# Optimization experiments

Measured on AMD Instinct MI355X. Metric: run time of the kernel, lower is better.

The kernel has to match this reference:

```python
import jax, jax.numpy as jnp
import numpy as np

DIM = 512
NUM_LATENTS = 128
TRUE_BATCH = 8
DOWNSCALING = 16


def setup_inputs() -> dict:
    key = jax.random.key(0)
    ks = jax.random.split(key, 7)
    B = TRUE_BATCH * NUM_LATENTS
    s = 0.02
    return {
        "x": jax.random.normal(ks[0], (B, DOWNSCALING, DIM), dtype=jnp.float32),
        "l": jax.random.normal(ks[1], (B, NUM_LATENTS, DIM), dtype=jnp.float32),
        "Wq": jax.random.normal(ks[2], (DIM, DIM), dtype=jnp.float32) * s,
        "Wk": jax.random.normal(ks[3], (DIM, DIM), dtype=jnp.float32) * s,
        "Wv": jax.random.normal(ks[4], (DIM, DIM), dtype=jnp.float32) * s,
        "Wo": jax.random.normal(ks[5], (DIM, DIM), dtype=jnp.float32) * s,
        "bo": jax.random.normal(ks[6], (DIM,), dtype=jnp.float32) * s,
        "num_heads": 8,
    }


def reference(x, l, Wq, Wk, Wv, Wo, bo, num_heads):
    B, n_tok, d = x.shape
    num_latents = l.shape[1]
    dh = d // num_heads

    def split_heads(t):
        # (b, n, h*d) -> (b, h, n, d)
        b, n, _ = t.shape
        return t.reshape(b, n, num_heads, dh).transpose(0, 2, 1, 3)

    q = split_heads(x @ Wq.T)   # (B, h, n_tok, dh)
    k = split_heads(l @ Wk.T)   # (B, h, num_latents, dh)
    v = split_heads(l @ Wv.T)

    scores = jnp.einsum('bhid,bhjd->bhij', q, k) * (dh ** -0.5)

    # mask row for batch element b is row (b mod num_latents) of a causal triu mask:
    # latent index m may attend only to latents j <= m.
    row = jnp.arange(B) % num_latents                       # (B,)
    allowed = jnp.arange(num_latents)[None, :] <= row[:, None]  # (B, num_latents)
    mask = jnp.where(allowed, 0.0, -jnp.inf).astype(scores.dtype)

    scores = scores + mask[:, None, None, :]
    attn = jax.nn.softmax(scores, axis=-1)

    out = jnp.einsum('bhij,bhjd->bhid', attn, v)            # (B, h, n_tok, dh)
    out = out.transpose(0, 2, 1, 3).reshape(B, n_tok, d)
    return out @ Wo.T + bo
```

## Files before the change

### kernel.cpp

```cpp
#include <hip/hip_runtime.h>


typedef __bf16 bf16;
typedef __attribute__((ext_vector_type(8))) __bf16 bf16x8;
typedef __attribute__((ext_vector_type(4))) __bf16 bf16x4;
typedef __attribute__((ext_vector_type(4))) float  float4v;

#define MFMA16(a, b, c) __builtin_amdgcn_mfma_f32_16x16x32_bf16((a), (b), (c), 0, 0, 0)

__device__ __forceinline__ void gl2lds16(const bf16* g, bf16* l) {
    __builtin_amdgcn_global_load_lds(
        (const __attribute__((address_space(1))) void*)g,
        (__attribute__((address_space(3))) void*)l, 16, 0, 0);
}

__global__ __launch_bounds__(256) void cast_f32_bf16(const float* __restrict__ src,
                                                     bf16* __restrict__ dst, int n4) {
    const int stride = gridDim.x * 256;
    for (int i = blockIdx.x * 256 + threadIdx.x; i < n4; i += stride) {
        float4v f = ((const float4v*)src)[i];
        ((bf16x4*)dst)[i] = bf16x4{(bf16)f.x, (bf16)f.y, (bf16)f.z, (bf16)f.w};
    }
}

__global__ __launch_bounds__(256) void cast_weights(const float* __restrict__ Wq,
                                                    const float* __restrict__ Wk,
                                                    const float* __restrict__ Wv,
                                                    const float* __restrict__ Wo,
                                                    bf16* __restrict__ Wq_b,
                                                    bf16* __restrict__ Wkv_b,
                                                    bf16* __restrict__ Wo_b) {
    const int i = blockIdx.x * 256 + threadIdx.x;
    const int w = i >> 16;
    const int j = i & 65535;
    const float* src = (w == 0) ? Wq : (w == 1) ? Wk : (w == 2) ? Wv : Wo;
    bf16x4* dst = (w == 0) ? (bf16x4*)Wq_b
                : (w == 1) ? (bf16x4*)Wkv_b
                : (w == 2) ? ((bf16x4*)Wkv_b) + 65536
                           : (bf16x4*)Wo_b;
    float4v f = ((const float4v*)src)[j];
    dst[j] = bf16x4{(bf16)f.x, (bf16)f.y, (bf16)f.z, (bf16)f.w};
}

template <int MODE>
__global__ __launch_bounds__(256) void gemm_bt(const bf16* __restrict__ A,
                                               const bf16* __restrict__ W,
                                               void* __restrict__ C0,
                                               const float* __restrict__ bias,
                                               int nT, int mPerXcd) {
    __shared__ alignas(16) bf16 Asl[128 * 32];
    __shared__ alignas(16) bf16 Bsl[128 * 32];

    const int bid = blockIdx.x;
    const int xcd = bid & 7;
    const int s   = bid >> 3;
    const int mt  = xcd * mPerXcd + s / nT;
    const int nt  = s % nT;
    const int m0  = mt * 128;
    const int n0  = nt * 128;

    const int tid  = threadIdx.x;
    const int wave = tid >> 6;
    const int lane = tid & 63;
    const int mi   = lane & 15;
    const int quad = lane >> 4;
    const int qrow = (wave >> 1) * 64;
    const int qcol = (wave & 1) * 64;

    const int srow = wave * 16 + (lane >> 2);
    const int scol = (lane & 3) * 8;

    float4v acc[4][4] = {};

    for (int kt = 0; kt < 16; ++kt) {
        const int k0 = kt * 32;
#pragma unroll
        for (int r = 0; r < 2; ++r) {
            gl2lds16(A + (size_t)(m0 + srow + r * 64) * 512 + k0 + scol,
                     &Asl[wave * 512 + r * 2048]);
            gl2lds16(W + (size_t)(n0 + srow + r * 64) * 512 + k0 + scol,
                     &Bsl[wave * 512 + r * 2048]);
        }
        __syncthreads();

        bf16x8 af[4], bfr[4];
#pragma unroll
        for (int i = 0; i < 4; ++i)
            af[i] = *(const bf16x8*)&Asl[(qrow + i * 16 + mi) * 32 + quad * 8];
#pragma unroll
        for (int j = 0; j < 4; ++j)
            bfr[j] = *(const bf16x8*)&Bsl[(qcol + j * 16 + mi) * 32 + quad * 8];
#pragma unroll
        for (int i = 0; i < 4; ++i)
#pragma unroll
            for (int j = 0; j < 4; ++j)
                acc[i][j] = MFMA16(af[i], bfr[j], acc[i][j]);
        __syncthreads();
    }

#pragma unroll
    for (int i = 0; i < 4; ++i) {
#pragma unroll
        for (int j = 0; j < 4; ++j) {
            const int row = m0 + qrow + i * 16 + quad * 4;
            const int col = n0 + qcol + j * 16 + mi;
#pragma unroll
            for (int r = 0; r < 4; ++r) {
                float v = acc[i][j][r];
                if (MODE == 2)
                    ((float*)C0)[(size_t)(row + r) * 512 + col] = v + bias[col];
                else
                    ((bf16*)C0)[(size_t)(row + r) * 512 + col] = (bf16)v;
            }
        }
    }
}

__global__ __launch_bounds__(512, 2) void gemm_kv(const bf16* __restrict__ A,
                                                  const bf16* __restrict__ W,
                                                  bf16* __restrict__ Kout,
                                                  bf16* __restrict__ Vt) {
    __shared__ alignas(16) bf16 As[4][256 * 32];
    __shared__ alignas(16) bf16 Bs[4][256 * 32];

    const int bid = blockIdx.x;
    const int xcd = bid & 7;
    const int s   = bid >> 3;
    const int mt  = xcd * 64 + (s >> 2);
    const int nt  = s & 3;
    const int m0  = mt * 256;
    const int n0  = nt * 256;

    const int tid  = threadIdx.x;
    const int wv   = tid >> 6;
    const int lane = tid & 63;
    const int wm   = wv >> 2;
    const int wn   = wv & 3;
    const int mi   = lane & 15;
    const int quad = lane >> 4;

    const int srow  = lane >> 2;
    const int sunit = (lane & 3) ^ (srow & 3);
    const bf16* gA = A + (size_t)(m0 + wv * 32 + srow) * 512 + sunit * 8;
    const bf16* gB = W + (size_t)(n0 + wv * 32 + srow) * 512 + sunit * 8;
    const int ldsOff0 = (wv * 32) * 32;
    const int ldsOff1 = ldsOff0 + 16 * 32;

    const int funit = (quad ^ (mi & 3)) * 8;
    const int arow0 = wm * 128 + mi;
    const int brow0 = wn * 64 + mi;

    float4v acc[8][4] = {};

#define KV_STAGE(t, ph)                                                        \
    do {                                                                       \
        const int _sl = (t) & 3;                                               \
        gl2lds16(gA + (ph) * (16 * 512) + (t) * 32,                            \
                 &As[_sl][(ph) ? ldsOff1 : ldsOff0]);                          \
        gl2lds16(gB + (ph) * (16 * 512) + (t) * 32,                            \
                 &Bs[_sl][(ph) ? ldsOff1 : ldsOff0]);                          \
    } while (0)

#pragma unroll
    for (int t = 0; t < 3; ++t) { KV_STAGE(t, 0); KV_STAGE(t, 1); }
    asm volatile("s_waitcnt vmcnt(8)" ::: "memory");
    asm volatile("s_barrier" ::: "memory");

    bf16x8 bfr[4];
#pragma unroll
    for (int t = 0; t < 16; ++t) {
        const int sl = t & 3;
#pragma unroll
        for (int mh = 0; mh < 2; ++mh) {
            bf16x8 af[4];
#pragma unroll
            for (int ii = 0; ii < 4; ++ii)
                af[ii] = *(const bf16x8*)
                    &As[sl][(arow0 + mh * 64 + ii * 16) * 32 + funit];
            if (mh == 0) {
#pragma unroll
                for (int j = 0; j < 4; ++j)
                    bfr[j] = *(const bf16x8*)&Bs[sl][(brow0 + j * 16) * 32 + funit];
            }
            if (t < 13) KV_STAGE(t + 3, mh);

            asm volatile("s_barrier" ::: "memory");
            asm volatile("s_waitcnt lgkmcnt(0)" ::: "memory");
            __builtin_amdgcn_s_setprio(1);
#pragma unroll
            for (int ii = 0; ii < 4; ++ii)
#pragma unroll
                for (int j = 0; j < 4; ++j)
                    acc[mh * 4 + ii][j] = MFMA16(af[ii], bfr[j], acc[mh * 4 + ii][j]);
            __builtin_amdgcn_s_setprio(0);

            if (mh == 1) {
                if (t <= 12)      asm volatile("s_waitcnt vmcnt(8)" ::: "memory");
                else if (t == 13) asm volatile("s_waitcnt vmcnt(4)" ::: "memory");
                else if (t == 14) asm volatile("s_waitcnt vmcnt(0)" ::: "memory");
            }
            asm volatile("s_barrier" ::: "memory");
        }
    }
#undef KV_STAGE

    if (nt < 2) {
#pragma unroll
        for (int i = 0; i < 8; ++i) {
            const int row = m0 + wm * 128 + i * 16 + quad * 4;
#pragma unroll
            for (int j = 0; j < 4; ++j) {
                const int col = n0 + wn * 64 + j * 16 + mi;
#pragma unroll
                for (int r = 0; r < 4; ++r)
                    Kout[(size_t)(row + r) * 512 + col] = (bf16)acc[i][j][r];
            }
        }
    } else {
        const size_t b = (size_t)mt * 2 + wm;
#pragma unroll
        for (int i = 0; i < 8; ++i) {
            const int lat0 = i * 16 + quad * 4;
#pragma unroll
            for (int j = 0; j < 4; ++j) {
                const int dd = (n0 - 512) + wn * 64 + j * 16 + mi;
                bf16x4 o = {(bf16)acc[i][j][0], (bf16)acc[i][j][1],
                            (bf16)acc[i][j][2], (bf16)acc[i][j][3]};
                *(bf16x4*)(Vt + (b * 512 + dd) * 128 + lat0) = o;
            }
        }
    }
}

__global__ __launch_bounds__(256) void attn_kernel(const bf16* __restrict__ Q,
                                                   const bf16* __restrict__ K,
                                                   const bf16* __restrict__ Vt,
                                                   bf16* __restrict__ O) {
    __shared__ alignas(16) bf16 Plds[4][16 * 136];

    const int w      = threadIdx.x >> 6;
    const int bh     = blockIdx.x * 4 + w;
    const int b      = bh >> 3;
    const int h      = bh & 7;
    const int rowb   = b & 127;
    const int ntiles = (rowb >> 4) + 1;
    const int nkt    = (ntiles + 1) >> 1;
    const int lane   = threadIdx.x & 63;
    const int mi     = lane & 15;
    const int quad   = lane >> 4;

    const bf16* qbase = Q + (size_t)(b * 16 + mi) * 512 + h * 64 + quad * 8;
    const bf16x8 aq0 = *(const bf16x8*)(qbase);
    const bf16x8 aq1 = *(const bf16x8*)(qbase + 32);

    float4v sc[8];
    const bf16* kbase = K + (size_t)(b * 128 + mi) * 512 + h * 64 + quad * 8;
#pragma unroll
    for (int jt = 0; jt < 8; ++jt) {
        if (jt < ntiles) {
            const bf16* kb = kbase + (size_t)jt * 16 * 512;
            bf16x8 bk0 = *(const bf16x8*)(kb);
            bf16x8 bk1 = *(const bf16x8*)(kb + 32);
            float4v a = {};
            a = MFMA16(aq0, bk0, a);
            a = MFMA16(aq1, bk1, a);
            sc[jt] = a;
        }
    }

#pragma unroll
    for (int jt = 0; jt < 8; ++jt) {
        if (jt < ntiles) {
            const bool masked = (jt * 16 + mi) > rowb;
#pragma unroll
            for (int r = 0; r < 4; ++r)
                sc[jt][r] = masked ? -1e30f : sc[jt][r] * 0.125f;
        }
    }

#pragma unroll
    for (int r = 0; r < 4; ++r) {
        float mx = sc[0][r];
#pragma unroll
        for (int jt = 1; jt < 8; ++jt)
            if (jt < ntiles) mx = fmaxf(mx, sc[jt][r]);
#pragma unroll
        for (int off = 1; off < 16; off <<= 1) mx = fmaxf(mx, __shfl_xor(mx, off, 64));
        float s = 0.f;
#pragma unroll
        for (int jt = 0; jt < 8; ++jt) {
            if (jt < ntiles) {
                float p = __expf(sc[jt][r] - mx);
                sc[jt][r] = p;
                s += p;
            }
        }
#pragma unroll
        for (int off = 1; off < 16; off <<= 1) s += __shfl_xor(s, off, 64);
        const float inv = 1.f / s;
#pragma unroll
        for (int jt = 0; jt < 8; ++jt) {
            if (jt < 2 * nkt) {
                float p = (jt < ntiles) ? sc[jt][r] * inv : 0.f;
                Plds[w][(quad * 4 + r) * 136 + jt * 16 + mi] = (bf16)p;
            }
        }
    }
    __syncthreads();

    float4v ao[4] = {};
    const bf16* vb0 = Vt + ((size_t)b * 512 + h * 64) * 128;
#pragma unroll
    for (int ks = 0; ks < 4; ++ks) {
        if (ks < nkt) {
            bf16x8 ap = *(const bf16x8*)&Plds[w][mi * 136 + ks * 32 + quad * 8];
#pragma unroll
            for (int jt = 0; jt < 4; ++jt) {
                bf16x8 bv = *(const bf16x8*)(vb0 + (size_t)(jt * 16 + mi) * 128
                                             + ks * 32 + quad * 8);
                ao[jt] = MFMA16(ap, bv, ao[jt]);
            }
        }
    }

#pragma unroll
    for (int jt = 0; jt < 4; ++jt)
#pragma unroll
        for (int r = 0; r < 4; ++r)
            O[(size_t)(b * 16 + quad * 4 + r) * 512 + h * 64 + jt * 16 + mi] =
                (bf16)ao[jt][r];
}

extern "C" void kernel_launch(void* const* d_in, const int* in_sizes, int n_in,
                              void* d_out, int out_size, void* d_ws, size_t ws_size,
                              hipStream_t stream) {
    const float* x  = (const float*)d_in[0];
    const float* l  = (const float*)d_in[1];
    const float* Wq = (const float*)d_in[2];
    const float* Wk = (const float*)d_in[3];
    const float* Wv = (const float*)d_in[4];
    const float* Wo = (const float*)d_in[5];
    const float* bo = (const float*)d_in[6];

    char* ws = (char*)d_ws;
    size_t off = 0;
    bf16* Wq_b  = (bf16*)(ws + off); off += (size_t)512 * 512 * 2;
    bf16* Wo_b  = (bf16*)(ws + off); off += (size_t)512 * 512 * 2;
    bf16* Wkv_b = (bf16*)(ws + off); off += (size_t)1024 * 512 * 2;
    bf16* xb    = (bf16*)(ws + off); off += (size_t)16384 * 512 * 2;
    bf16* lb    = (bf16*)(ws + off); off += (size_t)131072 * 512 * 2;
    bf16* Qb    = (bf16*)(ws + off); off += (size_t)16384 * 512 * 2;
    bf16* Kb    = (bf16*)(ws + off); off += (size_t)131072 * 512 * 2;
    bf16* Vtb   = (bf16*)(ws + off); off += (size_t)1024 * 512 * 128 * 2;
    bf16* AOb   = (bf16*)(ws + off);

    cast_weights<<<1024, 256, 0, stream>>>(Wq, Wk, Wv, Wo, Wq_b, Wkv_b, Wo_b);
    cast_f32_bf16<<<2048, 256, 0, stream>>>(x, xb, 16384 * 512 / 4);
    cast_f32_bf16<<<8192, 256, 0, stream>>>(l, lb, 131072 * 512 / 4);

    gemm_bt<0><<<512, 256, 0, stream>>>(xb, Wq_b, Qb, nullptr, 4, 16);
    gemm_kv<<<2048, 512, 0, stream>>>(lb, Wkv_b, Kb, Vtb);

    attn_kernel<<<2048, 256, 0, stream>>>(Qb, Kb, Vtb, AOb);

    gemm_bt<2><<<512, 256, 0, stream>>>(AOb, Wo_b, d_out, bo, 4, 16);
}
```

Before: 718.9 us.

## Stage KV GEMM epilogue through LDS for coalesced 16-byte stores; adjust swizzle

The K/V projection epilogue now writes accumulators into shared memory (reusing the pipeline buffers) one half-tile at a time. It then stores them to global memory as coalesced 16-byte vectors, replacing scattered 2-byte and 8-byte stores. The LDS swizzle pattern is also changed to use different row bits, which should reduce bank conflicts on the fragment reads. The cost is extra barriers and LDS traffic in the epilogue.

```diff
diff --git a/kernel.cpp b/kernel.cpp
--- a/kernel.cpp
+++ b/kernel.cpp
@@ -120,8 +120,7 @@
                                                   const bf16* __restrict__ W,
                                                   bf16* __restrict__ Kout,
                                                   bf16* __restrict__ Vt) {
-    __shared__ alignas(16) bf16 As[4][256 * 32];
-    __shared__ alignas(16) bf16 Bs[4][256 * 32];
+    __shared__ alignas(16) bf16 SH[2][4][256 * 32];
 
     const int bid = blockIdx.x;
     const int xcd = bid & 7;
@@ -140,13 +139,13 @@
     const int quad = lane >> 4;
 
     const int srow  = lane >> 2;
-    const int sunit = (lane & 3) ^ (srow & 3);
+    const int sunit = (lane & 3) ^ ((lane >> 3) & 3);
     const bf16* gA = A + (size_t)(m0 + wv * 32 + srow) * 512 + sunit * 8;
     const bf16* gB = W + (size_t)(n0 + wv * 32 + srow) * 512 + sunit * 8;
     const int ldsOff0 = (wv * 32) * 32;
     const int ldsOff1 = ldsOff0 + 16 * 32;
 
-    const int funit = (quad ^ (mi & 3)) * 8;
+    const int funit = (quad ^ ((mi >> 1) & 3)) * 8;
     const int arow0 = wm * 128 + mi;
     const int brow0 = wn * 64 + mi;
 
@@ -156,9 +155,9 @@
     do {                                                                       \
         const int _sl = (t) & 3;                                               \
         gl2lds16(gA + (ph) * (16 * 512) + (t) * 32,                            \
-                 &As[_sl][(ph) ? ldsOff1 : ldsOff0]);                          \
+                 &SH[0][_sl][(ph) ? ldsOff1 : ldsOff0]);                       \
         gl2lds16(gB + (ph) * (16 * 512) + (t) * 32,                            \
-                 &Bs[_sl][(ph) ? ldsOff1 : ldsOff0]);                          \
+                 &SH[1][_sl][(ph) ? ldsOff1 : ldsOff0]);                       \
     } while (0)
 
 #pragma unroll
@@ -176,11 +175,12 @@
 #pragma unroll
             for (int ii = 0; ii < 4; ++ii)
                 af[ii] = *(const bf16x8*)
-                    &As[sl][(arow0 + mh * 64 + ii * 16) * 32 + funit];
+                    &SH[0][sl][(arow0 + mh * 64 + ii * 16) * 32 + funit];
             if (mh == 0) {
 #pragma unroll
                 for (int j = 0; j < 4; ++j)
-                    bfr[j] = *(const bf16x8*)&Bs[sl][(brow0 + j * 16) * 32 + funit];
+                    bfr[j] = *(const bf16x8*)
+                        &SH[1][sl][(brow0 + j * 16) * 32 + funit];
             }
             if (t < 13) KV_STAGE(t + 3, mh);
 
@@ -204,29 +204,57 @@
     }
 #undef KV_STAGE
 
+    bf16* EP = &SH[0][0][0];
+
     if (nt < 2) {
 #pragma unroll
-        for (int i = 0; i < 8; ++i) {
-            const int row = m0 + wm * 128 + i * 16 + quad * 4;
-#pragma unroll
-            for (int j = 0; j < 4; ++j) {
-                const int col = n0 + wn * 64 + j * 16 + mi;
-#pragma unroll
-                for (int r = 0; r < 4; ++r)
-                    Kout[(size_t)(row + r) * 512 + col] = (bf16)acc[i][j][r];
+        for (int half = 0; half < 2; ++half) {
+            __syncthreads();
+            if (wm == half) {
+#pragma unroll
+                for (int i = 0; i < 8; ++i)
+#pragma unroll
+                    for (int j = 0; j < 4; ++j) {
+                        const int col = wn * 64 + j * 16 + mi;
+#pragma unroll
+                        for (int r = 0; r < 4; ++r)
+                            EP[(i * 16 + quad * 4 + r) * 264 + col] =
+                                (bf16)acc[i][j][r];
+                    }
+            }
+            __syncthreads();
+#pragma unroll
+            for (int rr = 0; rr < 8; ++rr) {
+                const int row_l = rr * 16 + (tid >> 5);
+                const int c8    = (tid & 31) * 8;
+                *(bf16x8*)&Kout[(size_t)(m0 + half * 128 + row_l) * 512 + n0 + c8] =
+                    *(const bf16x8*)&EP[row_l * 264 + c8];
             }
         }
     } else {
-        const size_t b = (size_t)mt * 2 + wm;
-#pragma unroll
-        for (int i = 0; i < 8; ++i) {
-            const int lat0 = i * 16 + quad * 4;
-#pragma unroll
-            for (int j = 0; j < 4; ++j) {
-                const int dd = (n0 - 512) + wn * 64 + j * 16 + mi;
-                bf16x4 o = {(bf16)acc[i][j][0], (bf16)acc[i][j][1],
-                            (bf16)acc[i][j][2], (bf16)acc[i][j][3]};
-                *(bf16x4*)(Vt + (b * 512 + dd) * 128 + lat0) = o;
+#pragma unroll
+        for (int half = 0; half < 2; ++half) {
+            __syncthreads();
+            if (wm == half) {
+#pragma unroll
+                for (int i = 0; i < 8; ++i)
+#pragma unroll
+                    for (int j = 0; j < 4; ++j) {
+                        const int dd_l = wn * 64 + j * 16 + mi;
+                        const int lat0 = i * 16 + quad * 4;
+                        *(bf16x4*)&EP[dd_l * 132 + lat0] =
+                            bf16x4{(bf16)acc[i][j][0], (bf16)acc[i][j][1],
+                                   (bf16)acc[i][j][2], (bf16)acc[i][j][3]};
+                    }
+            }
+            __syncthreads();
+            const size_t b = (size_t)mt * 2 + half;
+#pragma unroll
+            for (int rr = 0; rr < 8; ++rr) {
+                const int dd_l = rr * 32 + (tid >> 4);
+                const int l8   = (tid & 15) * 8;
+                *(bf16x8*)&Vt[(b * 512 + (n0 - 512) + dd_l) * 128 + l8] =
+                    *(const bf16x8*)&EP[dd_l * 132 + l8];
             }
         }
     }
```

Measured after the change: 683.3 us. 5.0% less time.
